# Kernel optimization log

Measured on AMD Instinct MI355X. Metric: run time of the kernel, lower is better.

Reference implementation:

```python
import jax, jax.numpy as jnp
import numpy as np

# nn.LSTMCell semantics, gate order: input, forget, cell(g), output

def setup_inputs() -> dict:
    key = jax.random.key(0)
    ks = jax.random.split(key, 7)
    T, B, I, H = 64, 512, 512, 1024
    s = 1.0 / np.sqrt(H)
    input_ = jax.random.normal(ks[0], (T, B, I), dtype=jnp.float32)
    ranges = jax.random.randint(ks[1], (B,), 0, T, dtype=jnp.int64)
    lengths = jax.random.randint(ks[2], (B,), 0, T, dtype=jnp.int64)
    W_ih = jax.random.uniform(ks[3], (4 * H, I), jnp.float32, -s, s)
    W_hh = jax.random.uniform(ks[4], (4 * H, H), jnp.float32, -s, s)
    b_ih = jax.random.uniform(ks[5], (4 * H,), jnp.float32, -s, s)
    b_hh = jax.random.uniform(ks[6], (4 * H,), jnp.float32, -s, s)
    return {"input_": input_, "ranges": ranges, "lengths": lengths,
            "W_ih": W_ih, "W_hh": W_hh, "b_ih": b_ih, "b_hh": b_hh}


def _lstm_forward(input_, W_ih, W_hh, b_ih, b_hh):
    T, B, _ = input_.shape
    H = W_hh.shape[1]
    # Precompute input-to-gate projections for all steps: [T, B, 4H]
    x_gates = jnp.einsum('tbi,gi->tbg', input_, W_ih) + b_ih + b_hh

    def step(carry, xg):
        h, c = carry
        gates = xg + h @ W_hh.T  # [B, 4H]
        i, f, g, o = jnp.split(gates, 4, axis=-1)
        i = jax.nn.sigmoid(i)
        f = jax.nn.sigmoid(f)
        g = jnp.tanh(g)
        o = jax.nn.sigmoid(o)
        c_next = f * c + i * g
        h_next = o * jnp.tanh(c_next)
        return (h_next, c_next), h_next

    h0 = jnp.zeros((B, H), dtype=input_.dtype)
    (h_n, c_n), hs = jax.lax.scan(step, (h0, h0), x_gates)
    # torch.cat(output, 0) of T tensors [B, H] -> [T*B, H]
    output = hs.reshape(T * B, H)
    return output, (h_n, c_n)


def reference(input_, ranges, lengths, W_ih, W_hh, b_ih, b_hh):
    # ranges/lengths are accepted but unused, matching the source module
    return _lstm_forward(input_, W_ih, W_hh, b_ih, b_hh)
```

## Files before the change

### kernel.cpp

```cpp
#include <hip/hip_runtime.h>

#define TT  64
#define BSZ 512
#define ISZ 512
#define HSZ 1024

typedef short bf16x8 __attribute__((ext_vector_type(8)));
typedef float f32x4 __attribute__((ext_vector_type(4)));
typedef unsigned short u16x8 __attribute__((ext_vector_type(8)));

typedef const __attribute__((address_space(1))) unsigned int* gas_t;
typedef __attribute__((address_space(3))) unsigned int* las_t;

__device__ __forceinline__ unsigned short f2bf(float f) {
    unsigned int u = __float_as_uint(f);
    unsigned int r = u + 0x7FFFu + ((u >> 16) & 1u);
    return (unsigned short)(r >> 16);
}
__device__ __forceinline__ float bf2f(unsigned short u) {
    return __uint_as_float(((unsigned int)u) << 16);
}

__global__ void cast_f32_to_bf16(const float* __restrict__ in,
                                 unsigned short* __restrict__ out, int n8) {
    int i = blockIdx.x * blockDim.x + threadIdx.x;
    if (i >= n8) return;
    const float4* p = (const float4*)(in + (size_t)i * 8);
    float4 v0 = p[0], v1 = p[1];
    u16x8 o;
    o[0] = f2bf(v0.x); o[1] = f2bf(v0.y); o[2] = f2bf(v0.z); o[3] = f2bf(v0.w);
    o[4] = f2bf(v1.x); o[5] = f2bf(v1.y); o[6] = f2bf(v1.z); o[7] = f2bf(v1.w);
    *(u16x8*)(out + (size_t)i * 8) = o;
}

__global__ void bias_combine(const float* __restrict__ a,
                             const float* __restrict__ b,
                             float* __restrict__ o) {
    int i = blockIdx.x * blockDim.x + threadIdx.x;
    if (i < 4 * HSZ) o[i] = a[i] + b[i];
}

__global__ __launch_bounds__(256) void xg_gemm(
    const unsigned short* __restrict__ xb,
    const unsigned short* __restrict__ Wihb,
    const float* __restrict__ bias,
    unsigned short* __restrict__ XG)
{
    __shared__ unsigned short Ab[2][128 * 64];
    __shared__ unsigned short Wb[2][128 * 64];

    const int t   = blockIdx.x >> 7;
    const int j   = blockIdx.x & 127;
    const int xcd = j & 7;
    const int idx = j >> 3;
    const int hh0 = (xcd * 4 + (idx & 3)) * 32;
    const int bb0 = (idx >> 2) * 128;

    const unsigned short* A = xb + (size_t)t * BSZ * ISZ;

    const int lane = threadIdx.x & 63;
    const int wv   = threadIdx.x >> 6;
    const int wx   = wv & 1;
    const int wy   = wv >> 1;
    const int lr   = lane & 15;
    const int kq   = lane >> 4;

    const f32x4 z = {0.f, 0.f, 0.f, 0.f};
    f32x4 acc[4][4];
    #pragma unroll
    for (int m = 0; m < 4; ++m)
        #pragma unroll
        for (int g = 0; g < 4; ++g) acc[m][g] = z;

    auto stage = [&](int k0, unsigned short* Abuf, unsigned short* Wbuf) {
        const int sub = lane >> 3;
        const int swk = ((lane & 7) ^ sub) * 8;
        #pragma unroll
        for (int i = 0; i < 4; ++i) {
            const int tr8 = (wv * 4 + i) * 8;
            const unsigned short* g = A + (size_t)(bb0 + tr8 + sub) * ISZ + k0 + swk;
            __builtin_amdgcn_global_load_lds((gas_t)g, (las_t)(Abuf + tr8 * 64), 16, 0, 0);
        }
        #pragma unroll
        for (int i = 0; i < 4; ++i) {
            const int tr8 = (wv * 4 + i) * 8;
            const int tr = tr8 + sub;
            const int wrow = hh0 + (tr & 31) + (tr >> 5) * 1024;
            const unsigned short* g = Wihb + (size_t)wrow * ISZ + k0 + swk;
            __builtin_amdgcn_global_load_lds((gas_t)g, (las_t)(Wbuf + tr8 * 64), 16, 0, 0);
        }
    };

    stage(0, Ab[0], Wb[0]);
    const int swz = (lr & 7) << 4;
    for (int c = 0; c < 8; ++c) {
        const int buf = c & 1;
        if (c + 1 < 8) {
            stage((c + 1) * 64, Ab[buf ^ 1], Wb[buf ^ 1]);
            asm volatile("s_waitcnt vmcnt(8)" ::: "memory");
        } else {
            asm volatile("s_waitcnt vmcnt(0)" ::: "memory");
        }
        __builtin_amdgcn_sched_barrier(0);
        __builtin_amdgcn_s_barrier();

        const char* Ac = (const char*)Ab[buf];
        const char* Wc = (const char*)Wb[buf];
        #pragma unroll
        for (int ks = 0; ks < 2; ++ks) {
            const int kb = ks * 64 + kq * 16;
            bf16x8 wf[4], af[4];
            #pragma unroll
            for (int g = 0; g < 4; ++g) {
                const int tr = g * 32 + wx * 16 + lr;
                wf[g] = *(const bf16x8*)(Wc + tr * 128 + (kb ^ swz));
            }
            #pragma unroll
            for (int m = 0; m < 4; ++m) {
                const int tr = wy * 64 + m * 16 + lr;
                af[m] = *(const bf16x8*)(Ac + tr * 128 + (kb ^ swz));
            }
            #pragma unroll
            for (int m = 0; m < 4; ++m)
                #pragma unroll
                for (int g = 0; g < 4; ++g)
                    acc[m][g] = __builtin_amdgcn_mfma_f32_16x16x32_bf16(af[m], wf[g], acc[m][g], 0, 0, 0);
        }
        __builtin_amdgcn_s_barrier();
    }

    const int n = hh0 + wx * 16 + lr;
    float bv[4];
    #pragma unroll
    for (int g = 0; g < 4; ++g) bv[g] = bias[g * HSZ + n];
    unsigned short* XGt = XG + (size_t)t * (4 * 64 * 8192);
    const size_t slab = ((size_t)(bb0 >> 7) * 64 + (n >> 4)) * 8192;
    #pragma unroll
    for (int m = 0; m < 4; ++m) {
        const int tid_c = ((m & 1) * 4 + wy * 2 + (m >> 1)) * 64 + kq * 16 + lr;
        u16x8 o0, o1;
        #pragma unroll
        for (int g = 0; g < 4; ++g)
            #pragma unroll
            for (int r = 0; r < 4; ++r) {
                const unsigned short v = f2bf(acc[m][g][r] + bv[g]);
                if (g < 2) o0[g * 4 + r] = v;
                else       o1[(g - 2) * 4 + r] = v;
            }
        *(u16x8*)(XGt + slab + (size_t)tid_c * 16) = o0;
        *(u16x8*)(XGt + slab + (size_t)tid_c * 16 + 8) = o1;
    }
}

__global__ __launch_bounds__(512, 2) void lstm_step(
    const unsigned short* __restrict__ XG,
    const unsigned short* __restrict__ Whhb,
    const unsigned short* __restrict__ hprev,
    unsigned short* __restrict__ hnext,
    float* __restrict__ cst,
    float* __restrict__ out,
    int t)
{
    __shared__ unsigned short WhL[64 * 1024];
    __shared__ float WS[4096];

    const int tid  = threadIdx.x;
    const int lane = tid & 63;
    const int wv   = tid >> 6;
    const int mg   = wv & 3;
    const int ks   = wv >> 2;
    const int lr   = lane & 15;
    const int kq   = lane >> 4;
    const int mi   = blockIdx.x >> 6;
    const int ni   = blockIdx.x & 63;
    const int b0   = mi * 128;
    const int hc0  = ni * 16;

    const int bth = b0 + mg * 32 + ks * 16 + kq * 4;
    const int n   = hc0 + lr;
    const unsigned short* xgt = XG + (size_t)t * 2097152
                              + ((size_t)mi * 64 + ni) * 8192 + (size_t)tid * 16;
    float* cth = cst + (((size_t)mi * 64 + ni) * 512 + tid) * 4;

    f32x4 accf[4];
    f32x4 cr;
    bf16x8 xg0, xg1;

    if (t > 0) {
        #pragma unroll
        for (int i = 0; i < 16; ++i) {
            const int li = wv * 16 + i;
            const int r = li >> 1, half = li & 1;
            const int grow = (r >> 4) * HSZ + hc0 + (r & 15);
            const int gslot = (half * 64 + lane) ^ (r & 7);
            const unsigned short* g = Whhb + (size_t)grow * HSZ + (size_t)gslot * 8;
            __builtin_amdgcn_global_load_lds((gas_t)g, (las_t)(WhL + li * 512), 16, 0, 0);
        }
        __builtin_amdgcn_sched_barrier(0);

        const int br0 = b0 + mg * 32 + lr;
        bf16x8 a0[2][8], a1[2][8];
        #pragma unroll
        for (int c = 0; c < 8; ++c) {
            const int kc = ks * 512 + c * 32 + kq * 8;
            const size_t base = (size_t)(kc >> 4) * 8192 + (kc & 15);
            a0[0][c] = *(const bf16x8*)(hprev + base + (size_t)br0 * 16);
            a0[1][c] = *(const bf16x8*)(hprev + base + (size_t)(br0 + 16) * 16);
        }
        __builtin_amdgcn_sched_barrier(0);
        #pragma unroll
        for (int c = 0; c < 8; ++c) {
            const int kc = ks * 512 + (c + 8) * 32 + kq * 8;
            const size_t base = (size_t)(kc >> 4) * 8192 + (kc & 15);
            a1[0][c] = *(const bf16x8*)(hprev + base + (size_t)br0 * 16);
            a1[1][c] = *(const bf16x8*)(hprev + base + (size_t)(br0 + 16) * 16);
        }
        __builtin_amdgcn_sched_barrier(0);

        xg0 = *(const bf16x8*)(xgt);
        xg1 = *(const bf16x8*)(xgt + 8);
        cr  = *(const f32x4*)(cth);
        __builtin_amdgcn_sched_barrier(0);

        asm volatile("s_waitcnt vmcnt(35)" ::: "memory");
        __builtin_amdgcn_sched_barrier(0);
        __builtin_amdgcn_s_barrier();

        const f32x4 z = {0.f, 0.f, 0.f, 0.f};
        f32x4 acc[2][4];
        #pragma unroll
        for (int m = 0; m < 2; ++m)
            #pragma unroll
            for (int g = 0; g < 4; ++g) acc[m][g] = z;

        asm volatile("s_waitcnt vmcnt(19)" ::: "memory");
        __builtin_amdgcn_sched_barrier(0);
        #pragma unroll
        for (int c = 0; c < 8; ++c) {
            const int u0 = ks * 64 + c * 4 + kq;
            const int woff = ((u0 ^ (lr & 7)) << 4);
            #pragma unroll
            for (int g = 0; g < 4; ++g) {
                bf16x8 wf = *(const bf16x8*)((const char*)WhL + (g * 16 + lr) * 2048 + woff);
                acc[0][g] = __builtin_amdgcn_mfma_f32_16x16x32_bf16(a0[0][c], wf, acc[0][g], 0, 0, 0);
                acc[1][g] = __builtin_amdgcn_mfma_f32_16x16x32_bf16(a0[1][c], wf, acc[1][g], 0, 0, 0);
            }
        }
        __builtin_amdgcn_sched_barrier(0);
        asm volatile("s_waitcnt vmcnt(3)" ::: "memory");
        __builtin_amdgcn_sched_barrier(0);
        #pragma unroll
        for (int c = 0; c < 8; ++c) {
            const int u0 = ks * 64 + (c + 8) * 4 + kq;
            const int woff = ((u0 ^ (lr & 7)) << 4);
            #pragma unroll
            for (int g = 0; g < 4; ++g) {
                bf16x8 wf = *(const bf16x8*)((const char*)WhL + (g * 16 + lr) * 2048 + woff);
                acc[0][g] = __builtin_amdgcn_mfma_f32_16x16x32_bf16(a1[0][c], wf, acc[0][g], 0, 0, 0);
                acc[1][g] = __builtin_amdgcn_mfma_f32_16x16x32_bf16(a1[1][c], wf, acc[1][g], 0, 0, 0);
            }
        }

        if (ks == 1) {
            #pragma unroll
            for (int g = 0; g < 4; ++g)
                *(f32x4*)&WS[mg * 1024 + g * 256 + lane * 4] = acc[0][g];
        }
        __syncthreads();
        if (ks == 0) {
            #pragma unroll
            for (int g = 0; g < 4; ++g)
                accf[g] = acc[0][g] + *(const f32x4*)&WS[mg * 1024 + g * 256 + lane * 4];
        }
        __syncthreads();
        if (ks == 0) {
            #pragma unroll
            for (int g = 0; g < 4; ++g)
                *(f32x4*)&WS[mg * 1024 + g * 256 + lane * 4] = acc[1][g];
        }
        __syncthreads();
        if (ks == 1) {
            #pragma unroll
            for (int g = 0; g < 4; ++g)
                accf[g] = acc[1][g] + *(const f32x4*)&WS[mg * 1024 + g * 256 + lane * 4];
        }
    } else {
        xg0 = *(const bf16x8*)(xgt);
        xg1 = *(const bf16x8*)(xgt + 8);
        cr  = (f32x4){0.f, 0.f, 0.f, 0.f};
        #pragma unroll
        for (int g = 0; g < 4; ++g) accf[g] = (f32x4){0.f, 0.f, 0.f, 0.f};
    }

    unsigned short* hslab = hnext + (size_t)ni * 8192;
    float* outt = out + (size_t)t * BSZ * HSZ;
    float* hnp = out + (size_t)TT * BSZ * HSZ;
    float* cnp = hnp + (size_t)BSZ * HSZ;
    #pragma unroll
    for (int r = 0; r < 4; ++r) {
        float gi = accf[0][r] + bf2f((unsigned short)xg0[r]);
        float gf = accf[1][r] + bf2f((unsigned short)xg0[4 + r]);
        float gg = accf[2][r] + bf2f((unsigned short)xg1[r]);
        float go = accf[3][r] + bf2f((unsigned short)xg1[4 + r]);
        float ig = 1.f / (1.f + __expf(-gi));
        float fg = 1.f / (1.f + __expf(-gf));
        float gv = 1.f - 2.f / (__expf(2.f * gg) + 1.f);
        float og = 1.f / (1.f + __expf(-go));
        float cnew = fg * cr[r] + ig * gv;
        float h = og * (1.f - 2.f / (__expf(2.f * cnew) + 1.f));
        cr[r] = cnew;
        const size_t idx = (size_t)(bth + r) * HSZ + n;
        hslab[(size_t)(bth + r) * 16 + lr] = f2bf(h);
        outt[idx] = h;
        if (t == TT - 1) { hnp[idx] = h; cnp[idx] = cnew; }
    }
    *(f32x4*)cth = cr;
}

extern "C" void kernel_launch(void* const* d_in, const int* in_sizes, int n_in,
                              void* d_out, int out_size, void* d_ws, size_t ws_size,
                              hipStream_t stream) {
    const float* input_ = (const float*)d_in[0];
    const float* Wih = (const float*)d_in[3];
    const float* Whh = (const float*)d_in[4];
    const float* bih = (const float*)d_in[5];
    const float* bhh = (const float*)d_in[6];

    char* ws = (char*)d_ws;
    unsigned short* Wihb = (unsigned short*)(ws);
    unsigned short* Whhb = (unsigned short*)(ws + (4u << 20));
    unsigned short* xb   = (unsigned short*)(ws + (12u << 20));
    float*          bias = (float*)(ws + (44u << 20));
    unsigned short* hb0  = (unsigned short*)(ws + (45u << 20));
    unsigned short* hb1  = (unsigned short*)(ws + (46u << 20));
    float*          cst  = (float*)(ws + (47u << 20));
    unsigned short* XG   = (unsigned short*)(ws + (50u << 20));

    cast_f32_to_bf16<<<1024, 256, 0, stream>>>(Wih, Wihb, (4 * HSZ * ISZ) / 8);
    cast_f32_to_bf16<<<2048, 256, 0, stream>>>(Whh, Whhb, (4 * HSZ * HSZ) / 8);
    cast_f32_to_bf16<<<8192, 256, 0, stream>>>(input_, xb, (TT * BSZ * ISZ) / 8);
    bias_combine<<<16, 256, 0, stream>>>(bih, bhh, bias);

    float* out = (float*)d_out;
    xg_gemm<<<TT * 128, 256, 0, stream>>>(xb, Wihb, bias, XG);
    for (int t = 0; t < TT; ++t) {
        const unsigned short* hp = (t & 1) ? hb0 : hb1;
        unsigned short* hx = (t & 1) ? hb1 : hb0;
        lstm_step<<<256, 512, 0, stream>>>(XG, Whhb, hp, hx, cst, out, t);
    }
}
```

Before: 920.0 us.

## Fuse input projection GEMM into per-step LSTM kernel, drop XG buffer

New measurement: 1.334 ms. 1.45x slower.

```diff
diff --git a/kernel.cpp b/kernel.cpp
--- a/kernel.cpp
+++ b/kernel.cpp
@@ -16,9 +16,6 @@
     unsigned int u = __float_as_uint(f);
     unsigned int r = u + 0x7FFFu + ((u >> 16) & 1u);
     return (unsigned short)(r >> 16);
-}
-__device__ __forceinline__ float bf2f(unsigned short u) {
-    return __uint_as_float(((unsigned int)u) << 16);
 }
 
 __global__ void cast_f32_to_bf16(const float* __restrict__ in,
@@ -40,121 +37,11 @@
     if (i < 4 * HSZ) o[i] = a[i] + b[i];
 }
 
-__global__ __launch_bounds__(256) void xg_gemm(
+__global__ __launch_bounds__(512, 2) void lstm_step(
     const unsigned short* __restrict__ xb,
     const unsigned short* __restrict__ Wihb,
+    const unsigned short* __restrict__ Whhb,
     const float* __restrict__ bias,
-    unsigned short* __restrict__ XG)
-{
-    __shared__ unsigned short Ab[2][128 * 64];
-    __shared__ unsigned short Wb[2][128 * 64];
-
-    const int t   = blockIdx.x >> 7;
-    const int j   = blockIdx.x & 127;
-    const int xcd = j & 7;
-    const int idx = j >> 3;
-    const int hh0 = (xcd * 4 + (idx & 3)) * 32;
-    const int bb0 = (idx >> 2) * 128;
-
-    const unsigned short* A = xb + (size_t)t * BSZ * ISZ;
-
-    const int lane = threadIdx.x & 63;
-    const int wv   = threadIdx.x >> 6;
-    const int wx   = wv & 1;
-    const int wy   = wv >> 1;
-    const int lr   = lane & 15;
-    const int kq   = lane >> 4;
-
-    const f32x4 z = {0.f, 0.f, 0.f, 0.f};
-    f32x4 acc[4][4];
-    #pragma unroll
-    for (int m = 0; m < 4; ++m)
-        #pragma unroll
-        for (int g = 0; g < 4; ++g) acc[m][g] = z;
-
-    auto stage = [&](int k0, unsigned short* Abuf, unsigned short* Wbuf) {
-        const int sub = lane >> 3;
-        const int swk = ((lane & 7) ^ sub) * 8;
-        #pragma unroll
-        for (int i = 0; i < 4; ++i) {
-            const int tr8 = (wv * 4 + i) * 8;
-            const unsigned short* g = A + (size_t)(bb0 + tr8 + sub) * ISZ + k0 + swk;
-            __builtin_amdgcn_global_load_lds((gas_t)g, (las_t)(Abuf + tr8 * 64), 16, 0, 0);
-        }
-        #pragma unroll
-        for (int i = 0; i < 4; ++i) {
-            const int tr8 = (wv * 4 + i) * 8;
-            const int tr = tr8 + sub;
-            const int wrow = hh0 + (tr & 31) + (tr >> 5) * 1024;
-            const unsigned short* g = Wihb + (size_t)wrow * ISZ + k0 + swk;
-            __builtin_amdgcn_global_load_lds((gas_t)g, (las_t)(Wbuf + tr8 * 64), 16, 0, 0);
-        }
-    };
-
-    stage(0, Ab[0], Wb[0]);
-    const int swz = (lr & 7) << 4;
-    for (int c = 0; c < 8; ++c) {
-        const int buf = c & 1;
-        if (c + 1 < 8) {
-            stage((c + 1) * 64, Ab[buf ^ 1], Wb[buf ^ 1]);
-            asm volatile("s_waitcnt vmcnt(8)" ::: "memory");
-        } else {
-            asm volatile("s_waitcnt vmcnt(0)" ::: "memory");
-        }
-        __builtin_amdgcn_sched_barrier(0);
-        __builtin_amdgcn_s_barrier();
-
-        const char* Ac = (const char*)Ab[buf];
-        const char* Wc = (const char*)Wb[buf];
-        #pragma unroll
-        for (int ks = 0; ks < 2; ++ks) {
-            const int kb = ks * 64 + kq * 16;
-            bf16x8 wf[4], af[4];
-            #pragma unroll
-            for (int g = 0; g < 4; ++g) {
-                const int tr = g * 32 + wx * 16 + lr;
-                wf[g] = *(const bf16x8*)(Wc + tr * 128 + (kb ^ swz));
-            }
-            #pragma unroll
-            for (int m = 0; m < 4; ++m) {
-                const int tr = wy * 64 + m * 16 + lr;
-                af[m] = *(const bf16x8*)(Ac + tr * 128 + (kb ^ swz));
-            }
-            #pragma unroll
-            for (int m = 0; m < 4; ++m)
-                #pragma unroll
-                for (int g = 0; g < 4; ++g)
-                    acc[m][g] = __builtin_amdgcn_mfma_f32_16x16x32_bf16(af[m], wf[g], acc[m][g], 0, 0, 0);
-        }
-        __builtin_amdgcn_s_barrier();
-    }
-
-    const int n = hh0 + wx * 16 + lr;
-    float bv[4];
-    #pragma unroll
-    for (int g = 0; g < 4; ++g) bv[g] = bias[g * HSZ + n];
-    unsigned short* XGt = XG + (size_t)t * (4 * 64 * 8192);
-    const size_t slab = ((size_t)(bb0 >> 7) * 64 + (n >> 4)) * 8192;
-    #pragma unroll
-    for (int m = 0; m < 4; ++m) {
-        const int tid_c = ((m & 1) * 4 + wy * 2 + (m >> 1)) * 64 + kq * 16 + lr;
-        u16x8 o0, o1;
-        #pragma unroll
-        for (int g = 0; g < 4; ++g)
-            #pragma unroll
-            for (int r = 0; r < 4; ++r) {
-                const unsigned short v = f2bf(acc[m][g][r] + bv[g]);
-                if (g < 2) o0[g * 4 + r] = v;
-                else       o1[(g - 2) * 4 + r] = v;
-            }
-        *(u16x8*)(XGt + slab + (size_t)tid_c * 16) = o0;
-        *(u16x8*)(XGt + slab + (size_t)tid_c * 16 + 8) = o1;
-    }
-}
-
-__global__ __launch_bounds__(512, 2) void lstm_step(
-    const unsigned short* __restrict__ XG,
-    const unsigned short* __restrict__ Whhb,
     const unsigned short* __restrict__ hprev,
     unsigned short* __restrict__ hnext,
     float* __restrict__ cst,
@@ -178,15 +65,22 @@
 
     const int bth = b0 + mg * 32 + ks * 16 + kq * 4;
     const int n   = hc0 + lr;
-    const unsigned short* xgt = XG + (size_t)t * 2097152
-                              + ((size_t)mi * 64 + ni) * 8192 + (size_t)tid * 16;
     float* cth = cst + (((size_t)mi * 64 + ni) * 512 + tid) * 4;
+
+    const unsigned short* xr = xb + (size_t)t * BSZ * ISZ
+                             + (size_t)(b0 + mg * 32 + lr) * ISZ + ks * 256 + kq * 8;
+    const unsigned short* wih_p = Wihb + (size_t)(hc0 + lr) * ISZ + ks * 256 + kq * 8;
 
     f32x4 accf[4];
     f32x4 cr;
-    bf16x8 xg0, xg1;
 
     if (t > 0) {
+        float bv[4];
+        #pragma unroll
+        for (int g = 0; g < 4; ++g) bv[g] = bias[g * HSZ + n];
+        cr = *(const f32x4*)(cth);
+        __builtin_amdgcn_sched_barrier(0);
+
         #pragma unroll
         for (int i = 0; i < 16; ++i) {
             const int li = wv * 16 + i;
@@ -198,8 +92,16 @@
         }
         __builtin_amdgcn_sched_barrier(0);
 
+        bf16x8 ax[2][8];
+        #pragma unroll
+        for (int j = 0; j < 8; ++j) {
+            ax[0][j] = *(const bf16x8*)(xr + j * 32);
+            ax[1][j] = *(const bf16x8*)(xr + 16 * ISZ + j * 32);
+        }
+        __builtin_amdgcn_sched_barrier(0);
+
         const int br0 = b0 + mg * 32 + lr;
-        bf16x8 a0[2][8], a1[2][8];
+        bf16x8 a0[2][8];
         #pragma unroll
         for (int c = 0; c < 8; ++c) {
             const int kc = ks * 512 + c * 32 + kq * 8;
@@ -208,6 +110,34 @@
             a0[1][c] = *(const bf16x8*)(hprev + base + (size_t)(br0 + 16) * 16);
         }
         __builtin_amdgcn_sched_barrier(0);
+
+        asm volatile("s_waitcnt vmcnt(32)" ::: "memory");
+        __builtin_amdgcn_sched_barrier(0);
+        __builtin_amdgcn_s_barrier();
+
+        asm volatile("s_waitcnt vmcnt(16)" ::: "memory");
+        __builtin_amdgcn_sched_barrier(0);
+
+        f32x4 acc[2][4];
+        #pragma unroll
+        for (int m = 0; m < 2; ++m)
+            #pragma unroll
+            for (int g = 0; g < 4; ++g)
+                acc[m][g] = (ks == 0) ? (f32x4){bv[g], bv[g], bv[g], bv[g]}
+                                      : (f32x4){0.f, 0.f, 0.f, 0.f};
+
+        #pragma unroll
+        for (int j = 0; j < 8; ++j) {
+            #pragma unroll
+            for (int g = 0; g < 4; ++g) {
+                bf16x8 wf = *(const bf16x8*)(wih_p + (size_t)g * (HSZ * ISZ) + j * 32);
+                acc[0][g] = __builtin_amdgcn_mfma_f32_16x16x32_bf16(ax[0][j], wf, acc[0][g], 0, 0, 0);
+                acc[1][g] = __builtin_amdgcn_mfma_f32_16x16x32_bf16(ax[1][j], wf, acc[1][g], 0, 0, 0);
+            }
+        }
+        __builtin_amdgcn_sched_barrier(0);
+
+        bf16x8 a1[2][8];
         #pragma unroll
         for (int c = 0; c < 8; ++c) {
             const int kc = ks * 512 + (c + 8) * 32 + kq * 8;
@@ -217,24 +147,6 @@
         }
         __builtin_amdgcn_sched_barrier(0);
 
-        xg0 = *(const bf16x8*)(xgt);
-        xg1 = *(const bf16x8*)(xgt + 8);
-        cr  = *(const f32x4*)(cth);
-        __builtin_amdgcn_sched_barrier(0);
-
-        asm volatile("s_waitcnt vmcnt(35)" ::: "memory");
-        __builtin_amdgcn_sched_barrier(0);
-        __builtin_amdgcn_s_barrier();
-
-        const f32x4 z = {0.f, 0.f, 0.f, 0.f};
-        f32x4 acc[2][4];
-        #pragma unroll
-        for (int m = 0; m < 2; ++m)
-            #pragma unroll
-            for (int g = 0; g < 4; ++g) acc[m][g] = z;
-
-        asm volatile("s_waitcnt vmcnt(19)" ::: "memory");
-        __builtin_amdgcn_sched_barrier(0);
         #pragma unroll
         for (int c = 0; c < 8; ++c) {
             const int u0 = ks * 64 + c * 4 + kq;
@@ -247,7 +159,7 @@
             }
         }
         __builtin_amdgcn_sched_barrier(0);
-        asm volatile("s_waitcnt vmcnt(3)" ::: "memory");
+        asm volatile("s_waitcnt vmcnt(0)" ::: "memory");
         __builtin_amdgcn_sched_barrier(0);
         #pragma unroll
         for (int c = 0; c < 8; ++c) {
@@ -285,11 +197,56 @@
                 accf[g] = acc[1][g] + *(const f32x4*)&WS[mg * 1024 + g * 256 + lane * 4];
         }
     } else {
-        xg0 = *(const bf16x8*)(xgt);
-        xg1 = *(const bf16x8*)(xgt + 8);
-        cr  = (f32x4){0.f, 0.f, 0.f, 0.f};
-        #pragma unroll
-        for (int g = 0; g < 4; ++g) accf[g] = (f32x4){0.f, 0.f, 0.f, 0.f};
+        float bv[4];
+        #pragma unroll
+        for (int g = 0; g < 4; ++g) bv[g] = bias[g * HSZ + n];
+        cr = (f32x4){0.f, 0.f, 0.f, 0.f};
+
+        f32x4 acc[2][4];
+        #pragma unroll
+        for (int m = 0; m < 2; ++m)
+            #pragma unroll
+            for (int g = 0; g < 4; ++g)
+                acc[m][g] = (ks == 0) ? (f32x4){bv[g], bv[g], bv[g], bv[g]}
+                                      : (f32x4){0.f, 0.f, 0.f, 0.f};
+        bf16x8 ax[2][8];
+        #pragma unroll
+        for (int j = 0; j < 8; ++j) {
+            ax[0][j] = *(const bf16x8*)(xr + j * 32);
+            ax[1][j] = *(const bf16x8*)(xr + 16 * ISZ + j * 32);
+        }
+        #pragma unroll
+        for (int j = 0; j < 8; ++j) {
+            #pragma unroll
+            for (int g = 0; g < 4; ++g) {
+                bf16x8 wf = *(const bf16x8*)(wih_p + (size_t)g * (HSZ * ISZ) + j * 32);
+                acc[0][g] = __builtin_amdgcn_mfma_f32_16x16x32_bf16(ax[0][j], wf, acc[0][g], 0, 0, 0);
+                acc[1][g] = __builtin_amdgcn_mfma_f32_16x16x32_bf16(ax[1][j], wf, acc[1][g], 0, 0, 0);
+            }
+        }
+        if (ks == 1) {
+            #pragma unroll
+            for (int g = 0; g < 4; ++g)
+                *(f32x4*)&WS[mg * 1024 + g * 256 + lane * 4] = acc[0][g];
+        }
+        __syncthreads();
+        if (ks == 0) {
+            #pragma unroll
+            for (int g = 0; g < 4; ++g)
+                accf[g] = acc[0][g] + *(const f32x4*)&WS[mg * 1024 + g * 256 + lane * 4];
+        }
+        __syncthreads();
+        if (ks == 0) {
+            #pragma unroll
+            for (int g = 0; g < 4; ++g)
+                *(f32x4*)&WS[mg * 1024 + g * 256 + lane * 4] = acc[1][g];
+        }
+        __syncthreads();
+        if (ks == 1) {
+            #pragma unroll
+            for (int g = 0; g < 4; ++g)
+                accf[g] = acc[1][g] + *(const f32x4*)&WS[mg * 1024 + g * 256 + lane * 4];
+        }
     }
 
     unsigned short* hslab = hnext + (size_t)ni * 8192;
@@ -298,10 +255,10 @@
     float* cnp = hnp + (size_t)BSZ * HSZ;
     #pragma unroll
     for (int r = 0; r < 4; ++r) {
-        float gi = accf[0][r] + bf2f((unsigned short)xg0[r]);
-        float gf = accf[1][r] + bf2f((unsigned short)xg0[4 + r]);
-        float gg = accf[2][r] + bf2f((unsigned short)xg1[r]);
-        float go = accf[3][r] + bf2f((unsigned short)xg1[4 + r]);
+        float gi = accf[0][r];
+        float gf = accf[1][r];
+        float gg = accf[2][r];
+        float go = accf[3][r];
         float ig = 1.f / (1.f + __expf(-gi));
         float fg = 1.f / (1.f + __expf(-gf));
         float gv = 1.f - 2.f / (__expf(2.f * gg) + 1.f);
@@ -334,7 +291,6 @@
     unsigned short* hb0  = (unsigned short*)(ws + (45u << 20));
     unsigned short* hb1  = (unsigned short*)(ws + (46u << 20));
     float*          cst  = (float*)(ws + (47u << 20));
-    unsigned short* XG   = (unsigned short*)(ws + (50u << 20));
 
     cast_f32_to_bf16<<<1024, 256, 0, stream>>>(Wih, Wihb, (4 * HSZ * ISZ) / 8);
     cast_f32_to_bf16<<<2048, 256, 0, stream>>>(Whh, Whhb, (4 * HSZ * HSZ) / 8);
@@ -342,10 +298,9 @@
     bias_combine<<<16, 256, 0, stream>>>(bih, bhh, bias);
 
     float* out = (float*)d_out;
-    xg_gemm<<<TT * 128, 256, 0, stream>>>(xb, Wihb, bias, XG);
     for (int t = 0; t < TT; ++t) {
         const unsigned short* hp = (t & 1) ? hb0 : hb1;
         unsigned short* hx = (t & 1) ? hb1 : hb0;
-        lstm_step<<<256, 512, 0, stream>>>(XG, Whhb, hp, hx, cst, out, t);
+        lstm_step<<<256, 512, 0, stream>>>(xb, Wihb, Whhb, bias, hp, hx, cst, out, t);
     }
 }
```

## Split batch rows across waves instead of splitting K, drop LDS reduction

Applied to the files above, without the earlier changes.

After: 951.3 us. 3.4% more time.

```diff
diff --git a/kernel.cpp b/kernel.cpp
--- a/kernel.cpp
+++ b/kernel.cpp
@@ -137,7 +137,7 @@
     const size_t slab = ((size_t)(bb0 >> 7) * 64 + (n >> 4)) * 8192;
     #pragma unroll
     for (int m = 0; m < 4; ++m) {
-        const int tid_c = ((m & 1) * 4 + wy * 2 + (m >> 1)) * 64 + kq * 16 + lr;
+        const int tid_c = (wy * 4 + m) * 64 + kq * 16 + lr;
         u16x8 o0, o1;
         #pragma unroll
         for (int g = 0; g < 4; ++g)
@@ -162,13 +162,10 @@
     int t)
 {
     __shared__ unsigned short WhL[64 * 1024];
-    __shared__ float WS[4096];
 
     const int tid  = threadIdx.x;
     const int lane = tid & 63;
     const int wv   = tid >> 6;
-    const int mg   = wv & 3;
-    const int ks   = wv >> 2;
     const int lr   = lane & 15;
     const int kq   = lane >> 4;
     const int mi   = blockIdx.x >> 6;
@@ -176,13 +173,15 @@
     const int b0   = mi * 128;
     const int hc0  = ni * 16;
 
-    const int bth = b0 + mg * 32 + ks * 16 + kq * 4;
+    const int bth = b0 + wv * 16 + kq * 4;
     const int n   = hc0 + lr;
     const unsigned short* xgt = XG + (size_t)t * 2097152
                               + ((size_t)mi * 64 + ni) * 8192 + (size_t)tid * 16;
     float* cth = cst + (((size_t)mi * 64 + ni) * 512 + tid) * 4;
 
-    f32x4 accf[4];
+    f32x4 acc[4];
+    #pragma unroll
+    for (int g = 0; g < 4; ++g) acc[g] = (f32x4){0.f, 0.f, 0.f, 0.f};
     f32x4 cr;
     bf16x8 xg0, xg1;
 
@@ -198,22 +197,20 @@
         }
         __builtin_amdgcn_sched_barrier(0);
 
-        const int br0 = b0 + mg * 32 + lr;
-        bf16x8 a0[2][8], a1[2][8];
-        #pragma unroll
-        for (int c = 0; c < 8; ++c) {
-            const int kc = ks * 512 + c * 32 + kq * 8;
+        const int br0 = b0 + wv * 16 + lr;
+        bf16x8 a0[16], a1[16];
+        #pragma unroll
+        for (int c = 0; c < 16; ++c) {
+            const int kc = c * 32 + kq * 8;
             const size_t base = (size_t)(kc >> 4) * 8192 + (kc & 15);
-            a0[0][c] = *(const bf16x8*)(hprev + base + (size_t)br0 * 16);
-            a0[1][c] = *(const bf16x8*)(hprev + base + (size_t)(br0 + 16) * 16);
-        }
-        __builtin_amdgcn_sched_barrier(0);
-        #pragma unroll
-        for (int c = 0; c < 8; ++c) {
-            const int kc = ks * 512 + (c + 8) * 32 + kq * 8;
+            a0[c] = *(const bf16x8*)(hprev + base + (size_t)br0 * 16);
+        }
+        __builtin_amdgcn_sched_barrier(0);
+        #pragma unroll
+        for (int c = 0; c < 16; ++c) {
+            const int kc = (c + 16) * 32 + kq * 8;
             const size_t base = (size_t)(kc >> 4) * 8192 + (kc & 15);
-            a1[0][c] = *(const bf16x8*)(hprev + base + (size_t)br0 * 16);
-            a1[1][c] = *(const bf16x8*)(hprev + base + (size_t)(br0 + 16) * 16);
+            a1[c] = *(const bf16x8*)(hprev + base + (size_t)br0 * 16);
         }
         __builtin_amdgcn_sched_barrier(0);
 
@@ -226,70 +223,35 @@
         __builtin_amdgcn_sched_barrier(0);
         __builtin_amdgcn_s_barrier();
 
-        const f32x4 z = {0.f, 0.f, 0.f, 0.f};
-        f32x4 acc[2][4];
-        #pragma unroll
-        for (int m = 0; m < 2; ++m)
-            #pragma unroll
-            for (int g = 0; g < 4; ++g) acc[m][g] = z;
-
         asm volatile("s_waitcnt vmcnt(19)" ::: "memory");
         __builtin_amdgcn_sched_barrier(0);
         #pragma unroll
-        for (int c = 0; c < 8; ++c) {
-            const int u0 = ks * 64 + c * 4 + kq;
+        for (int c = 0; c < 16; ++c) {
+            const int u0 = c * 4 + kq;
             const int woff = ((u0 ^ (lr & 7)) << 4);
             #pragma unroll
             for (int g = 0; g < 4; ++g) {
                 bf16x8 wf = *(const bf16x8*)((const char*)WhL + (g * 16 + lr) * 2048 + woff);
-                acc[0][g] = __builtin_amdgcn_mfma_f32_16x16x32_bf16(a0[0][c], wf, acc[0][g], 0, 0, 0);
-                acc[1][g] = __builtin_amdgcn_mfma_f32_16x16x32_bf16(a0[1][c], wf, acc[1][g], 0, 0, 0);
+                acc[g] = __builtin_amdgcn_mfma_f32_16x16x32_bf16(a0[c], wf, acc[g], 0, 0, 0);
             }
         }
         __builtin_amdgcn_sched_barrier(0);
         asm volatile("s_waitcnt vmcnt(3)" ::: "memory");
         __builtin_amdgcn_sched_barrier(0);
         #pragma unroll
-        for (int c = 0; c < 8; ++c) {
-            const int u0 = ks * 64 + (c + 8) * 4 + kq;
+        for (int c = 0; c < 16; ++c) {
+            const int u0 = (c + 16) * 4 + kq;
             const int woff = ((u0 ^ (lr & 7)) << 4);
             #pragma unroll
             for (int g = 0; g < 4; ++g) {
                 bf16x8 wf = *(const bf16x8*)((const char*)WhL + (g * 16 + lr) * 2048 + woff);
-                acc[0][g] = __builtin_amdgcn_mfma_f32_16x16x32_bf16(a1[0][c], wf, acc[0][g], 0, 0, 0);
-                acc[1][g] = __builtin_amdgcn_mfma_f32_16x16x32_bf16(a1[1][c], wf, acc[1][g], 0, 0, 0);
-            }
-        }
-
-        if (ks == 1) {
-            #pragma unroll
-            for (int g = 0; g < 4; ++g)
-                *(f32x4*)&WS[mg * 1024 + g * 256 + lane * 4] = acc[0][g];
-        }
-        __syncthreads();
-        if (ks == 0) {
-            #pragma unroll
-            for (int g = 0; g < 4; ++g)
-                accf[g] = acc[0][g] + *(const f32x4*)&WS[mg * 1024 + g * 256 + lane * 4];
-        }
-        __syncthreads();
-        if (ks == 0) {
-            #pragma unroll
-            for (int g = 0; g < 4; ++g)
-                *(f32x4*)&WS[mg * 1024 + g * 256 + lane * 4] = acc[1][g];
-        }
-        __syncthreads();
-        if (ks == 1) {
-            #pragma unroll
-            for (int g = 0; g < 4; ++g)
-                accf[g] = acc[1][g] + *(const f32x4*)&WS[mg * 1024 + g * 256 + lane * 4];
+                acc[g] = __builtin_amdgcn_mfma_f32_16x16x32_bf16(a1[c], wf, acc[g], 0, 0, 0);
+            }
         }
     } else {
         xg0 = *(const bf16x8*)(xgt);
         xg1 = *(const bf16x8*)(xgt + 8);
         cr  = (f32x4){0.f, 0.f, 0.f, 0.f};
-        #pragma unroll
-        for (int g = 0; g < 4; ++g) accf[g] = (f32x4){0.f, 0.f, 0.f, 0.f};
     }
 
     unsigned short* hslab = hnext + (size_t)ni * 8192;
@@ -298,10 +260,10 @@
     float* cnp = hnp + (size_t)BSZ * HSZ;
     #pragma unroll
     for (int r = 0; r < 4; ++r) {
-        float gi = accf[0][r] + bf2f((unsigned short)xg0[r]);
-        float gf = accf[1][r] + bf2f((unsigned short)xg0[4 + r]);
-        float gg = accf[2][r] + bf2f((unsigned short)xg1[r]);
-        float go = accf[3][r] + bf2f((unsigned short)xg1[4 + r]);
+        float gi = acc[0][r] + bf2f((unsigned short)xg0[r]);
+        float gf = acc[1][r] + bf2f((unsigned short)xg0[4 + r]);
+        float gg = acc[2][r] + bf2f((unsigned short)xg1[r]);
+        float go = acc[3][r] + bf2f((unsigned short)xg1[4 + r]);
         float ig = 1.f / (1.f + __expf(-gi));
         float fg = 1.f / (1.f + __expf(-gf));
         float gv = 1.f - 2.f / (__expf(2.f * gg) + 1.f);
```
